# Kernel tuning notes

Hardware: AMD Instinct MI355X
Metric: run time of the kernel (lower is better)

The kernel has to match this reference:

```python
import jax, jax.numpy as jnp
import numpy as np

NUM_HEADS = 12
SCALE = 1.0 / np.sqrt(768 // NUM_HEADS)  # 0.125


def setup_inputs() -> dict:
    key = jax.random.key(0)
    k1, k2, k3, k4, k5 = jax.random.split(key, 5)
    B, N, C = 4, 2048, 768
    x = jax.random.normal(k1, (B, N, C), dtype=jnp.float32)
    qkv_w = jax.random.normal(k2, (3 * C, C), dtype=jnp.float32) * 0.02
    qkv_b = jax.random.normal(k3, (3 * C,), dtype=jnp.float32) * 0.02
    proj_w = jax.random.normal(k4, (C, C), dtype=jnp.float32) * 0.02
    proj_b = jax.random.normal(k5, (C,), dtype=jnp.float32) * 0.02
    return {"x": x, "qkv_w": qkv_w, "qkv_b": qkv_b, "proj_w": proj_w, "proj_b": proj_b}


def reference(x, qkv_w, qkv_b, proj_w, proj_b):
    B, N, C = x.shape
    H = NUM_HEADS
    Dh = C // H
    # qkv projection (torch Linear: x @ W^T + b)
    qkv = x @ qkv_w.T + qkv_b                      # [B, N, 3C]
    qkv = qkv.reshape(B, N, 3, H, Dh).transpose(2, 0, 3, 1, 4)  # [3, B, H, N, Dh]
    q, k, v = qkv[0], qkv[1], qkv[2]
    q = q * SCALE
    attn = jnp.einsum("bhnd,bhmd->bhnm", q, k)     # [B, H, N, N]
    attn = jax.nn.softmax(attn, axis=-1)
    out = jnp.einsum("bhnm,bhmd->bhnd", attn, v)   # [B, H, N, Dh]
    out = out.transpose(0, 2, 1, 3).reshape(B, N, C)
    out = out @ proj_w.T + proj_b
    return out
```

## Files before the change

kernel.cpp:

```cpp
#include <hip/hip_runtime.h>
#include <math.h>

typedef __attribute__((ext_vector_type(8))) short short8;
typedef __attribute__((ext_vector_type(4))) float f32x4;
typedef __attribute__((ext_vector_type(16))) float f32x16;

namespace {

constexpr int B  = 4;
constexpr int N  = 2048;
constexpr int C  = 768;
constexpr int H  = 12;
constexpr int Dh = 64;
constexpr int M  = B * N;
constexpr int C3 = 3 * C;

constexpr float QSCALE = 0.125f * 1.4426950408889634f;

__device__ inline unsigned short f2bf(float x) {
  unsigned int u = __float_as_uint(x);
  return (unsigned short)((u + 0x7fffu + ((u >> 16) & 1u)) >> 16);
}

__device__ inline unsigned cvt_pk_bf16(float lo, float hi) {
  unsigned r;
  asm("v_cvt_pk_bf16_f32 %0, %1, %2" : "=v"(r) : "v"(lo), "v"(hi));
  return r;
}

__device__ inline void gload_lds16(const void* g, void* lds) {
  __builtin_amdgcn_global_load_lds(
      (const __attribute__((address_space(1))) void*)g,
      (__attribute__((address_space(3))) void*)lds, 16, 0, 0);
}

__device__ inline float max3f(float a, float b, float c) {
  return fmaxf(fmaxf(a, b), c);
}

__global__ __launch_bounds__(256) void cvt_f32_bf16(
    const float* __restrict__ in, unsigned short* __restrict__ out, int n4) {
  int i = blockIdx.x * 256 + threadIdx.x;
  if (i < n4) {
    float4 v = reinterpret_cast<const float4*>(in)[i];
    ushort4 o;
    o.x = f2bf(v.x); o.y = f2bf(v.y); o.z = f2bf(v.z); o.w = f2bf(v.w);
    reinterpret_cast<ushort4*>(out)[i] = o;
  }
}

template <bool QKV_EPI>
__global__ __launch_bounds__(256, 2) void gemm_mfma_bt(
    const unsigned short* __restrict__ A, const unsigned short* __restrict__ Bw,
    const float* __restrict__ bias, void* __restrict__ outp, int Nd, int K) {
  __shared__ alignas(16) unsigned short lA[128 * 64];
  __shared__ alignas(16) unsigned short lB[128 * 64];
  const int t = threadIdx.x, wave = t >> 6, lane = t & 63;
  const int bm = blockIdx.x * 128, bn = blockIdx.y * 128;
  const int wr = (wave >> 1) * 64, wc = (wave & 1) * 64;

  f32x4 acc[4][4];
#pragma unroll
  for (int i = 0; i < 4; ++i)
#pragma unroll
    for (int j = 0; j < 4; ++j) acc[i][j] = (f32x4){0.f, 0.f, 0.f, 0.f};

  const int srow = lane >> 3;
  const int scol = ((lane & 7) ^ srow) * 8;
  const int rb0  = wave * 32;

  for (int k0 = 0; k0 < K; k0 += 64) {
#pragma unroll
    for (int i = 0; i < 4; ++i) {
      const int rb = rb0 + i * 8;
      const unsigned short* ga = A  + (size_t)(bm + rb + srow) * K + k0 + scol;
      const unsigned short* gb = Bw + (size_t)(bn + rb + srow) * K + k0 + scol;
      gload_lds16(ga, (char*)lA + rb * 128);
      gload_lds16(gb, (char*)lB + rb * 128);
    }
    __syncthreads();

#pragma unroll
    for (int kc = 0; kc < 2; ++kc) {
      short8 af[4], bfr[4];
#pragma unroll
      for (int mt = 0; mt < 4; ++mt) {
        const int row = wr + mt * 16 + (lane & 15);
        const int q = (row * 128 + kc * 64 + (lane >> 4) * 16) ^ ((row & 7) << 4);
        af[mt] = *reinterpret_cast<const short8*>((const char*)lA + q);
      }
#pragma unroll
      for (int nt = 0; nt < 4; ++nt) {
        const int row = wc + nt * 16 + (lane & 15);
        const int q = (row * 128 + kc * 64 + (lane >> 4) * 16) ^ ((row & 7) << 4);
        bfr[nt] = *reinterpret_cast<const short8*>((const char*)lB + q);
      }
#pragma unroll
      for (int mt = 0; mt < 4; ++mt)
#pragma unroll
        for (int nt = 0; nt < 4; ++nt)
          acc[mt][nt] = __builtin_amdgcn_mfma_f32_16x16x32_bf16(
              af[mt], bfr[nt], acc[mt][nt], 0, 0, 0);
    }
    __syncthreads();
  }

  const int r0 = (lane >> 4) * 4;
  const int cl = lane & 15;
#pragma unroll
  for (int nt = 0; nt < 4; ++nt) {
    const int col = bn + wc + nt * 16 + cl;
    const float bs = bias[col];
    const float sc = (QKV_EPI && col < C) ? QSCALE : 1.0f;
#pragma unroll
    for (int mt = 0; mt < 4; ++mt) {
#pragma unroll
      for (int r = 0; r < 4; ++r) {
        const size_t row = bm + wr + mt * 16 + r0 + r;
        const float v = acc[mt][nt][r] + bs;
        if (QKV_EPI)
          ((unsigned short*)outp)[row * Nd + col] = f2bf(v * sc);
        else
          ((float*)outp)[row * Nd + col] = v;
      }
    }
  }
}

__global__ __launch_bounds__(256) void vt_prepass(
    const unsigned short* __restrict__ qkvbf, unsigned short* __restrict__ vt) {
  const int bh = blockIdx.x, b = bh / H, h = bh % H;
  const int nt = blockIdx.y;
  __shared__ unsigned short tile[64][72];
  const int t = threadIdx.x;
  const int r = t >> 2, ch = (t & 3) * 16;

  const unsigned short* src =
      qkvbf + (size_t)(b * N + nt * 64 + r) * C3 + 2 * C + h * Dh + ch;
  *reinterpret_cast<int4*>(&tile[r][ch])     = *reinterpret_cast<const int4*>(src);
  *reinterpret_cast<int4*>(&tile[r][ch + 8]) = *reinterpret_cast<const int4*>(src + 8);
  __syncthreads();

  alignas(16) unsigned short vals[16];
#pragma unroll
  for (int i = 0; i < 16; ++i) vals[i] = tile[ch + i][r];
  unsigned short* dst = vt + ((size_t)bh * Dh + r) * N + nt * 64 + ch;
  *reinterpret_cast<int4*>(dst)     = *reinterpret_cast<int4*>(&vals[0]);
  *reinterpret_cast<int4*>(dst + 8) = *reinterpret_cast<int4*>(&vals[8]);
}

__global__ __launch_bounds__(256) void attn_mfma32(
    const unsigned short* __restrict__ qkvbf,
    const unsigned short* __restrict__ vt,
    unsigned short* __restrict__ ctx) {
  const int bh = blockIdx.x, b = bh / H, h = bh % H;
  const int qt = blockIdx.y;
  const int t = threadIdx.x;
  const int wave = t >> 6, lane = t & 63;
  const int ql = lane & 31;
  const int hi = lane >> 5;
  const int q0 = qt * 128 + wave * 32;

  __shared__ alignas(16) char lds[2][16384];

  short8 qf[4];
  {
    const unsigned short* qrow =
        qkvbf + (size_t)(b * N + q0 + ql) * C3 + h * Dh + 8 * hi;
#pragma unroll
    for (int s = 0; s < 4; ++s) {
      int4 v = *reinterpret_cast<const int4*>(qrow + 16 * s);
      qf[s] = *reinterpret_cast<short8*>(&v);
    }
  }

  f32x16 ot0, ot1;
#pragma unroll
  for (int r = 0; r < 16; ++r) { ot0[r] = 0.f; ot1[r] = 0.f; }
  float mrun = -INFINITY, lrun = 0.f;

  const int rl = lane >> 3;
  const int cs = ((lane & 7) ^ rl) * 8;
  const size_t kgbase = (size_t)(b * N) * C3 + C + h * Dh;
  const unsigned short* kstg =
      qkvbf + kgbase + (size_t)(wave * 16 + rl) * C3 + cs;
  const unsigned short* vstg =
      vt + ((size_t)bh * Dh + wave * 16 + rl) * N + cs;

  auto stage = [&](char* bufc, int kt) {
    const unsigned short* kp = kstg + (size_t)(kt * 64) * C3;
    const unsigned short* vp = vstg + kt * 64;
    char* kd = bufc + (wave * 16) * 128;
    char* vd = bufc + 8192 + (wave * 16) * 128;
    gload_lds16(kp,          kd);
    gload_lds16(kp + 8 * C3, kd + 8 * 128);
    gload_lds16(vp,          vd);
    gload_lds16(vp + 8 * N,  vd + 8 * 128);
  };

  constexpr int NT = N / 64;

  auto kaddr = [&](int row, int s) {
    return (row * 128 + 32 * s + 16 * hi) ^ ((row & 7) << 4);
  };

  stage(lds[0], 0);
  __syncthreads();

  for (int kt = 0; kt < NT; ++kt) {
    char* bufc = lds[kt & 1];
    if (kt + 1 < NT) stage(lds[(kt + 1) & 1], kt + 1);

    f32x16 s0, s1;
#pragma unroll
    for (int r = 0; r < 16; ++r) { s0[r] = 0.f; s1[r] = 0.f; }
    __builtin_amdgcn_s_setprio(1);
#pragma unroll
    for (int s = 0; s < 4; ++s) {
      short8 k0 = *reinterpret_cast<const short8*>(bufc + kaddr(ql, s));
      short8 k1 = *reinterpret_cast<const short8*>(bufc + kaddr(32 + ql, s));
      s0 = __builtin_amdgcn_mfma_f32_32x32x16_bf16(k0, qf[s], s0, 0, 0, 0);
      s1 = __builtin_amdgcn_mfma_f32_32x32x16_bf16(k1, qf[s], s1, 0, 0, 0);
    }
    __builtin_amdgcn_s_setprio(0);

    short8 vf[8];
    const char* bufv = bufc + 8192;
#pragma unroll
    for (int s = 0; s < 4; ++s) {
      vf[2 * s]     = *reinterpret_cast<const short8*>(bufv + kaddr(ql, s));
      vf[2 * s + 1] = *reinterpret_cast<const short8*>(bufv + kaddr(32 + ql, s));
    }

    float t0 = max3f(s0[0], s0[1], s0[2]);
    float t1 = max3f(s0[3], s0[4], s0[5]);
    float t2 = max3f(s0[6], s0[7], s0[8]);
    float t3 = max3f(s0[9], s0[10], s0[11]);
    float t4 = max3f(s0[12], s0[13], s0[14]);
    float t5 = max3f(s0[15], s1[0], s1[1]);
    float t6 = max3f(s1[2], s1[3], s1[4]);
    float t7 = max3f(s1[5], s1[6], s1[7]);
    float t8 = max3f(s1[8], s1[9], s1[10]);
    float t9 = max3f(s1[11], s1[12], s1[13]);
    float ta = fmaxf(s1[14], s1[15]);
    t0 = max3f(t0, t1, t2);
    t3 = max3f(t3, t4, t5);
    t6 = max3f(t6, t7, t8);
    t9 = max3f(t9, ta, t0);
    const float mx = max3f(t3, t6, t9);
    if (!__all(mx <= mrun + 8.f)) {
      const float nm = fmaxf(mrun, fmaxf(mx, __shfl_xor(mx, 32)));
      const float corr = __builtin_amdgcn_exp2f(mrun - nm);
      lrun *= corr;
#pragma unroll
      for (int r = 0; r < 16; ++r) {
        const int qr = (r & 3) + 8 * (r >> 2) + 4 * hi;
        const float cr = __shfl(corr, qr);
        ot0[r] *= cr; ot1[r] *= cr;
      }
      mrun = nm;
    }

    short8 pf0, pf1, pf2, pf3;
    auto mkfrag = [&](const f32x16& sh, short8& fA, short8& fB) {
      float e[16];
#pragma unroll
      for (int r = 0; r < 16; ++r) e[r] = __builtin_amdgcn_exp2f(sh[r] - mrun);
      lrun += (((e[0] + e[1]) + (e[2] + e[3])) + ((e[4] + e[5]) + (e[6] + e[7]))) +
              (((e[8] + e[9]) + (e[10] + e[11])) + ((e[12] + e[13]) + (e[14] + e[15])));
      unsigned w[8];
#pragma unroll
      for (int tt = 0; tt < 4; ++tt) {
        w[2 * tt]     = cvt_pk_bf16(e[4 * tt], e[4 * tt + 1]);
        w[2 * tt + 1] = cvt_pk_bf16(e[4 * tt + 2], e[4 * tt + 3]);
      }
      unsigned a0 = w[0], a1 = w[1], b0 = w[2], b1 = w[3];
      asm("v_permlane32_swap_b32 %0, %1" : "+v"(a0), "+v"(b0));
      asm("v_permlane32_swap_b32 %0, %1" : "+v"(a1), "+v"(b1));
      int4 p0; p0.x = a0; p0.y = a1; p0.z = b0; p0.w = b1;
      fA = *reinterpret_cast<short8*>(&p0);
      unsigned c0 = w[4], c1 = w[5], d0 = w[6], d1 = w[7];
      asm("v_permlane32_swap_b32 %0, %1" : "+v"(c0), "+v"(d0));
      asm("v_permlane32_swap_b32 %0, %1" : "+v"(c1), "+v"(d1));
      int4 p1; p1.x = c0; p1.y = c1; p1.z = d0; p1.w = d1;
      fB = *reinterpret_cast<short8*>(&p1);
    };
    mkfrag(s0, pf0, pf1);
    mkfrag(s1, pf2, pf3);

    __builtin_amdgcn_s_setprio(1);
    ot0 = __builtin_amdgcn_mfma_f32_32x32x16_bf16(pf0, vf[0], ot0, 0, 0, 0);
    ot1 = __builtin_amdgcn_mfma_f32_32x32x16_bf16(pf0, vf[1], ot1, 0, 0, 0);
    ot0 = __builtin_amdgcn_mfma_f32_32x32x16_bf16(pf1, vf[2], ot0, 0, 0, 0);
    ot1 = __builtin_amdgcn_mfma_f32_32x32x16_bf16(pf1, vf[3], ot1, 0, 0, 0);
    ot0 = __builtin_amdgcn_mfma_f32_32x32x16_bf16(pf2, vf[4], ot0, 0, 0, 0);
    ot1 = __builtin_amdgcn_mfma_f32_32x32x16_bf16(pf2, vf[5], ot1, 0, 0, 0);
    ot0 = __builtin_amdgcn_mfma_f32_32x32x16_bf16(pf3, vf[6], ot0, 0, 0, 0);
    ot1 = __builtin_amdgcn_mfma_f32_32x32x16_bf16(pf3, vf[7], ot1, 0, 0, 0);
    __builtin_amdgcn_s_setprio(0);

    __syncthreads();
  }

  lrun += __shfl_xor(lrun, 32);
  const float inv = 1.f / lrun;
#pragma unroll
  for (int r = 0; r < 16; ++r) {
    const int qr = (r & 3) + 8 * (r >> 2) + 4 * hi;
    const float ir = __shfl(inv, qr);
    unsigned short* orow = ctx + (size_t)(b * N + q0 + qr) * C + h * Dh;
    orow[ql]      = f2bf(ot0[r] * ir);
    orow[32 + ql] = f2bf(ot1[r] * ir);
  }
}

}

extern "C" void kernel_launch(void* const* d_in, const int* in_sizes, int n_in,
                              void* d_out, int out_size, void* d_ws, size_t ws_size,
                              hipStream_t stream) {
  const float* x      = (const float*)d_in[0];
  const float* qkv_w  = (const float*)d_in[1];
  const float* qkv_b  = (const float*)d_in[2];
  const float* proj_w = (const float*)d_in[3];
  const float* proj_b = (const float*)d_in[4];
  float* out = (float*)d_out;

  unsigned short* qkvbf = (unsigned short*)d_ws;
  unsigned short* ctx   = qkvbf + (size_t)M * C3;
  unsigned short* vt    = ctx + (size_t)M * C;
  unsigned short* xbf   = vt + (size_t)M * C;
  unsigned short* wqkv  = xbf + (size_t)M * C;
  unsigned short* wproj = wqkv + (size_t)C3 * C;

  cvt_f32_bf16<<<(M * C / 4 + 255) / 256, 256, 0, stream>>>(x, xbf, M * C / 4);
  cvt_f32_bf16<<<(C3 * C / 4 + 255) / 256, 256, 0, stream>>>(qkv_w, wqkv, C3 * C / 4);
  cvt_f32_bf16<<<(C * C / 4 + 255) / 256, 256, 0, stream>>>(proj_w, wproj, C * C / 4);

  gemm_mfma_bt<true>
      <<<dim3(M / 128, C3 / 128), 256, 0, stream>>>(xbf, wqkv, qkv_b, qkvbf, C3, C);
  vt_prepass<<<dim3(B * H, N / 64), 256, 0, stream>>>(qkvbf, vt);
  attn_mfma32<<<dim3(B * H, N / 128), 256, 0, stream>>>(qkvbf, vt, ctx);
  gemm_mfma_bt<false>
      <<<dim3(M / 128, C / 128), 256, 0, stream>>>(ctx, wproj, proj_b, out, C, C);
}
```

Measured before the change: 147.3 us.

## Triple-buffer attention K/V staging and fuse fp32-to-bf16 conversion launches

```diff
diff --git a/kernel.cpp b/kernel.cpp
--- a/kernel.cpp
+++ b/kernel.cpp
@@ -38,14 +38,21 @@
   return fmaxf(fmaxf(a, b), c);
 }
 
-__global__ __launch_bounds__(256) void cvt_f32_bf16(
-    const float* __restrict__ in, unsigned short* __restrict__ out, int n4) {
-  int i = blockIdx.x * 256 + threadIdx.x;
-  if (i < n4) {
-    float4 v = reinterpret_cast<const float4*>(in)[i];
+__global__ __launch_bounds__(256) void cvt_all3(
+    const float* __restrict__ x, const float* __restrict__ qw,
+    const float* __restrict__ pw, unsigned short* __restrict__ xbf,
+    unsigned short* __restrict__ wqkv, unsigned short* __restrict__ wproj) {
+  constexpr int n1 = M * C / 4, n2 = C3 * C / 4, n3 = C * C / 4;
+  constexpr int tot = n1 + n2 + n3;
+  for (int i = blockIdx.x * 256 + threadIdx.x; i < tot; i += gridDim.x * 256) {
+    const float4* s; unsigned short* d; int j;
+    if (i < n1)            { s = (const float4*)x;  d = xbf;   j = i; }
+    else if (i < n1 + n2)  { s = (const float4*)qw; d = wqkv;  j = i - n1; }
+    else                   { s = (const float4*)pw; d = wproj; j = i - n1 - n2; }
+    float4 v = s[j];
     ushort4 o;
     o.x = f2bf(v.x); o.y = f2bf(v.y); o.z = f2bf(v.z); o.w = f2bf(v.w);
-    reinterpret_cast<ushort4*>(out)[i] = o;
+    reinterpret_cast<ushort4*>(d)[j] = o;
   }
 }
 
@@ -161,7 +168,7 @@
   const int hi = lane >> 5;
   const int q0 = qt * 128 + wave * 32;
 
-  __shared__ alignas(16) char lds[2][16384];
+  __shared__ alignas(16) char lds[3][16384];
 
   short8 qf[4];
   {
@@ -187,9 +194,10 @@
   const unsigned short* vstg =
       vt + ((size_t)bh * Dh + wave * 16 + rl) * N + cs;
 
-  auto stage = [&](char* bufc, int kt) {
-    const unsigned short* kp = kstg + (size_t)(kt * 64) * C3;
-    const unsigned short* vp = vstg + kt * 64;
+  auto stage = [&](int j) {
+    char* bufc = lds[j % 3];
+    const unsigned short* kp = kstg + (size_t)(j * 64) * C3;
+    const unsigned short* vp = vstg + j * 64;
     char* kd = bufc + (wave * 16) * 128;
     char* vd = bufc + 8192 + (wave * 16) * 128;
     gload_lds16(kp,          kd);
@@ -204,12 +212,18 @@
     return (row * 128 + 32 * s + 16 * hi) ^ ((row & 7) << 4);
   };
 
-  stage(lds[0], 0);
-  __syncthreads();
+  stage(0);
+  stage(1);
 
   for (int kt = 0; kt < NT; ++kt) {
-    char* bufc = lds[kt & 1];
-    if (kt + 1 < NT) stage(lds[(kt + 1) & 1], kt + 1);
+    if (kt < NT - 1) asm volatile("s_waitcnt vmcnt(4)" ::: "memory");
+    else             asm volatile("s_waitcnt vmcnt(0)" ::: "memory");
+    __builtin_amdgcn_s_barrier();
+    __builtin_amdgcn_sched_barrier(0);
+
+    if (kt + 2 < NT) stage(kt + 2);
+
+    const char* bufc = lds[kt % 3];
 
     f32x16 s0, s1;
 #pragma unroll
@@ -298,8 +312,6 @@
     ot0 = __builtin_amdgcn_mfma_f32_32x32x16_bf16(pf3, vf[6], ot0, 0, 0, 0);
     ot1 = __builtin_amdgcn_mfma_f32_32x32x16_bf16(pf3, vf[7], ot1, 0, 0, 0);
     __builtin_amdgcn_s_setprio(0);
-
-    __syncthreads();
   }
 
   lrun += __shfl_xor(lrun, 32);
@@ -333,9 +345,7 @@
   unsigned short* wqkv  = xbf + (size_t)M * C;
   unsigned short* wproj = wqkv + (size_t)C3 * C;
 
-  cvt_f32_bf16<<<(M * C / 4 + 255) / 256, 256, 0, stream>>>(x, xbf, M * C / 4);
-  cvt_f32_bf16<<<(C3 * C / 4 + 255) / 256, 256, 0, stream>>>(qkv_w, wqkv, C3 * C / 4);
-  cvt_f32_bf16<<<(C * C / 4 + 255) / 256, 256, 0, stream>>>(proj_w, wproj, C * C / 4);
+  cvt_all3<<<2048, 256, 0, stream>>>(x, qkv_w, proj_w, xbf, wqkv, wproj);
 
   gemm_mfma_bt<true>
       <<<dim3(M / 128, C3 / 128), 256, 0, stream>>>(xbf, wqkv, qkv_b, qkvbf, C3, C);
```

New measurement: 149.0 us. Within noise of the previous version (+1.1%).
